# Kernel tuning notes

Hardware: AMD Instinct MI355X
Metric: run time of the kernel (lower is better)

The kernel has to match this reference:

```python
import jax, jax.numpy as jnp
import numpy as np

N = 50000
E = 800000
NFEAT, NHID, NCODE, NCLASS = 512, 256, 64, 40


def setup_inputs() -> dict:
    key = jax.random.key(0)
    ks = jax.random.split(key, 16)
    def glorot(k, shape):
        lim = 1.0 / np.sqrt(shape[0])
        return jax.random.uniform(k, shape, jnp.float32, -lim, lim)
    return {
        "x": jax.random.normal(ks[0], (N, NFEAT), jnp.float32),
        "edge_src": jax.random.randint(ks[1], (E,), 0, N, jnp.int32),
        "edge_dst": jax.random.randint(ks[2], (E,), 0, N, jnp.int32),
        "edge_weight": jax.random.uniform(ks[3], (E,), jnp.float32),
        "eps": jax.random.normal(ks[4], (N, NCODE), jnp.float32),
        # gc1: GraphConvolution(nfeat, nhid)
        "W1": glorot(ks[5], (NFEAT, NHID)),
        "b1": glorot(ks[6], (NHID,)),
        # fc11 / fc12: Linear(nhid, ncode)
        "W_mu": glorot(ks[7], (NHID, NCODE)),
        "b_mu": glorot(ks[8], (NCODE,)),
        "W_lv": glorot(ks[9], (NHID, NCODE)),
        "b_lv": glorot(ks[10], (NCODE,)),
        # fc2: Linear(ncode, nhid)
        "W_dec": glorot(ks[11], (NCODE, NHID)),
        "b_dec": glorot(ks[12], (NHID,)),
        # gc2: GraphConvolution(2*nhid, nclass)
        "W2": glorot(ks[13], (2 * NHID, NCLASS)),
        "b2": glorot(ks[14], (NCLASS,)),
    }


def spmm(edge_src, edge_dst, edge_weight, support):
    # spmm(adj, support): gather rows at src, scale by edge weight, scatter-add to dst
    msgs = support[edge_src] * edge_weight[:, None]  # [E, d]
    return jax.ops.segment_sum(msgs, edge_dst, num_segments=N)


def reference(x, edge_src, edge_dst, edge_weight, eps,
              W1, b1, W_mu, b_mu, W_lv, b_lv, W_dec, b_dec, W2, b2):
    # gc1: relu(spmm(adj, x @ W1) + b1)
    h1 = jax.nn.relu(spmm(edge_src, edge_dst, edge_weight, x @ W1) + b1)
    # dropout is identity in inference mode
    mu = h1 @ W_mu + b_mu
    log_var = h1 @ W_lv + b_lv
    # reparametrize: std = exp(log_var) (as in source, no 0.5 factor)
    z = mu + eps * jnp.exp(log_var)
    # decode
    x1 = jax.nn.relu(z @ W_dec + b_dec)
    x1 = jnp.concatenate([x1, h1], axis=1)  # [N, 2*nhid]
    # gc2
    logits = spmm(edge_src, edge_dst, edge_weight, x1 @ W2) + b2
    return jax.nn.log_softmax(logits, axis=1)
```

## Files before the change

kernel.cpp:

```cpp
#include <hip/hip_runtime.h>
#include <math.h>

#define N_NODES 50000
#define N_EDGES 800000
#define NFEAT 512
#define NHID 256
#define NCODE 64
#define NCLASS 40
#define NCLS_PAD 48
#define NB_SCAN 196

typedef __attribute__((ext_vector_type(8))) short short8;
typedef __attribute__((ext_vector_type(8))) unsigned short ushort8;
typedef __attribute__((ext_vector_type(4))) unsigned short ushort4v;
typedef __attribute__((ext_vector_type(4))) float floatx4;

__device__ inline unsigned short f2bf(float f) {
    unsigned u = __builtin_bit_cast(unsigned, f);
    u += 0x7fff + ((u >> 16) & 1);
    return (unsigned short)(u >> 16);
}
__device__ inline float bf2f(unsigned short h) {
    return __builtin_bit_cast(float, (unsigned)h << 16);
}

__global__ __launch_bounds__(256) void hist_kernel(const int* __restrict__ dst,
                                                   int* __restrict__ counts) {
    int t = blockIdx.x * 256 + threadIdx.x;
    if (t < N_EDGES) atomicAdd(&counts[dst[t]], 1);
}

__global__ __launch_bounds__(256) void scan_block_sums(const int* __restrict__ counts,
                                                       int* __restrict__ blockSums) {
    __shared__ int red[256];
    int t = threadIdx.x;
    int i = blockIdx.x * 256 + t;
    red[t] = (i < N_NODES) ? counts[i] : 0;
    __syncthreads();
#pragma unroll
    for (int off = 128; off > 0; off >>= 1) {
        if (t < off) red[t] += red[t + off];
        __syncthreads();
    }
    if (t == 0) blockSums[blockIdx.x] = red[0];
}

__global__ __launch_bounds__(256) void scan_block_offsets(const int* __restrict__ blockSums,
                                                          int* __restrict__ blockOffsets,
                                                          int* __restrict__ offsets) {
    __shared__ int s[256];
    int t = threadIdx.x;
    int v = (t < NB_SCAN) ? blockSums[t] : 0;
    s[t] = v;
    __syncthreads();
#pragma unroll
    for (int off = 1; off < 256; off <<= 1) {
        int x = (t >= off) ? s[t - off] : 0;
        __syncthreads();
        s[t] += x;
        __syncthreads();
    }
    if (t < NB_SCAN) blockOffsets[t] = s[t] - v;
    if (t == 255) offsets[N_NODES] = s[255];
}

__global__ __launch_bounds__(256) void scan_final(const int* __restrict__ counts,
                                                  const int* __restrict__ blockOffsets,
                                                  int* __restrict__ offsets) {
    __shared__ int s[256];
    int t = threadIdx.x;
    int i = blockIdx.x * 256 + t;
    int v = (i < N_NODES) ? counts[i] : 0;
    s[t] = v;
    __syncthreads();
#pragma unroll
    for (int off = 1; off < 256; off <<= 1) {
        int x = (t >= off) ? s[t - off] : 0;
        __syncthreads();
        s[t] += x;
        __syncthreads();
    }
    if (i < N_NODES) offsets[i] = blockOffsets[blockIdx.x] + s[t] - v;
}

__global__ __launch_bounds__(256) void scatter_kernel(const int* __restrict__ dst,
                                                      const int* __restrict__ src,
                                                      const float* __restrict__ w,
                                                      const int* __restrict__ offsets,
                                                      int* __restrict__ cursor,
                                                      int2* __restrict__ edges) {
    int t = blockIdx.x * 256 + threadIdx.x;
    if (t < N_EDGES) {
        int d = dst[t];
        int pos = offsets[d] + atomicAdd(&cursor[d], 1);
        edges[pos] = make_int2(src[t], __builtin_bit_cast(int, w[t]));
    }
}

__global__ __launch_bounds__(256) void wprep_kernel(const float* __restrict__ W1,
                                                    const float* __restrict__ W2,
                                                    const float* __restrict__ W_mu,
                                                    const float* __restrict__ W_lv,
                                                    const float* __restrict__ W_dec,
                                                    unsigned short* __restrict__ W1t,
                                                    unsigned short* __restrict__ W2bt,
                                                    unsigned short* __restrict__ W_mulvt,
                                                    unsigned short* __restrict__ W_dect) {
    int idx = blockIdx.x * 256 + threadIdx.x;
    if (idx < NFEAT * NHID) {
        int k = idx >> 8;
        int n = idx & 255;
        W1t[(size_t)n * NFEAT + k] = f2bf(W1[idx]);
    } else if (idx < NFEAT * NHID + NCLS_PAD * NFEAT) {
        int i2 = idx - NFEAT * NHID;
        int n = i2 >> 9;
        int k = i2 & 511;
        W2bt[i2] = (n < NCLASS) ? f2bf(W2[(size_t)k * NCLASS + n]) : (unsigned short)0;
    } else if (idx < NFEAT * NHID + NCLS_PAD * NFEAT + 128 * 256) {
        int i2 = idx - NFEAT * NHID - NCLS_PAD * NFEAT;
        int j = i2 >> 8;
        int k = i2 & 255;
        float v = (j < 64) ? W_mu[(size_t)k * NCODE + j] : W_lv[(size_t)k * NCODE + (j - 64)];
        W_mulvt[i2] = f2bf(v);
    } else if (idx < NFEAT * NHID + NCLS_PAD * NFEAT + 128 * 256 + 256 * 64) {
        int i2 = idx - NFEAT * NHID - NCLS_PAD * NFEAT - 128 * 256;
        int n = i2 >> 6;
        int k = i2 & 63;
        W_dect[i2] = f2bf(W_dec[(size_t)k * NHID + n]);
    }
}

__global__ __launch_bounds__(256) void gemm1_mfma(const float* __restrict__ A,
                                                  const unsigned short* __restrict__ Bt,
                                                  unsigned short* __restrict__ C) {
    __shared__ unsigned short As[64][72];
    __shared__ unsigned short Bs[128][72];
    int t = threadIdx.x;
    int wave = t >> 6, lane = t & 63;
    int quad = lane >> 4, m16 = lane & 15;
    int m0 = blockIdx.x * 64;
    int n0 = blockIdx.y * 128;

    floatx4 acc[8];
#pragma unroll
    for (int i = 0; i < 8; i++) acc[i] = (floatx4){0.f, 0.f, 0.f, 0.f};

    int ar = t >> 2;
    int ako = (t & 3) * 16;
    int arow = m0 + ar;
    if (arow >= N_NODES) arow = N_NODES - 1;
    const float* Abase = A + (size_t)arow * NFEAT + ako;

    int bcol = t >> 1;
    int bko = (t & 1) * 32;
    const unsigned short* Bbase = Bt + (size_t)(n0 + bcol) * NFEAT + bko;

    for (int k0 = 0; k0 < NFEAT; k0 += 64) {
        float4 a0 = *(const float4*)(Abase + k0);
        float4 a1 = *(const float4*)(Abase + k0 + 4);
        float4 a2 = *(const float4*)(Abase + k0 + 8);
        float4 a3 = *(const float4*)(Abase + k0 + 12);
        ushort8 b0 = *(const ushort8*)(Bbase + k0);
        ushort8 b1 = *(const ushort8*)(Bbase + k0 + 8);
        ushort8 b2 = *(const ushort8*)(Bbase + k0 + 16);
        ushort8 b3 = *(const ushort8*)(Bbase + k0 + 24);
        __syncthreads();
        ushort8 av0, av1;
        av0[0] = f2bf(a0.x); av0[1] = f2bf(a0.y); av0[2] = f2bf(a0.z); av0[3] = f2bf(a0.w);
        av0[4] = f2bf(a1.x); av0[5] = f2bf(a1.y); av0[6] = f2bf(a1.z); av0[7] = f2bf(a1.w);
        av1[0] = f2bf(a2.x); av1[1] = f2bf(a2.y); av1[2] = f2bf(a2.z); av1[3] = f2bf(a2.w);
        av1[4] = f2bf(a3.x); av1[5] = f2bf(a3.y); av1[6] = f2bf(a3.z); av1[7] = f2bf(a3.w);
        *(ushort8*)&As[ar][ako] = av0;
        *(ushort8*)&As[ar][ako + 8] = av1;
        *(ushort8*)&Bs[bcol][bko] = b0;
        *(ushort8*)&Bs[bcol][bko + 8] = b1;
        *(ushort8*)&Bs[bcol][bko + 16] = b2;
        *(ushort8*)&Bs[bcol][bko + 24] = b3;
        __syncthreads();
#pragma unroll
        for (int c = 0; c < 2; c++) {
            short8 afrag = *(const short8*)&As[wave * 16 + m16][c * 32 + quad * 8];
#pragma unroll
            for (int nt = 0; nt < 8; nt++) {
                short8 bfrag = *(const short8*)&Bs[nt * 16 + m16][c * 32 + quad * 8];
                acc[nt] = __builtin_amdgcn_mfma_f32_16x16x32_bf16(afrag, bfrag, acc[nt], 0, 0, 0);
            }
        }
    }
#pragma unroll
    for (int nt = 0; nt < 8; nt++) {
        int col = n0 + nt * 16 + m16;
#pragma unroll
        for (int r = 0; r < 4; r++) {
            int row = m0 + wave * 16 + quad * 4 + r;
            if (row < N_NODES) C[(size_t)row * NHID + col] = f2bf(acc[nt][r]);
        }
    }
}

__global__ __launch_bounds__(256) void spmm1_kernel(const int* __restrict__ offsets,
                                                    const int2* __restrict__ edges,
                                                    const unsigned short* __restrict__ S1b,
                                                    const float* __restrict__ b1,
                                                    unsigned short* __restrict__ x1cat) {
    int n = blockIdx.x * 4 + (threadIdx.x >> 6);
    int lane = threadIdx.x & 63;
    int beg = offsets[n], end = offsets[n + 1];
    float ax = 0.f, ay = 0.f, az = 0.f, aw = 0.f;
    int i = beg;
    for (; i + 8 <= end; i += 8) {
        int2 e[8];
        ushort4v r[8];
#pragma unroll
        for (int u = 0; u < 8; u++) e[u] = edges[i + u];
#pragma unroll
        for (int u = 0; u < 8; u++)
            r[u] = *(const ushort4v*)&S1b[(size_t)e[u].x * NHID + lane * 4];
#pragma unroll
        for (int u = 0; u < 8; u++) {
            float ww = __builtin_bit_cast(float, e[u].y);
            ax += ww * bf2f(r[u][0]);
            ay += ww * bf2f(r[u][1]);
            az += ww * bf2f(r[u][2]);
            aw += ww * bf2f(r[u][3]);
        }
    }
    for (; i < end; i++) {
        int2 e = edges[i];
        float ww = __builtin_bit_cast(float, e.y);
        ushort4v r = *(const ushort4v*)&S1b[(size_t)e.x * NHID + lane * 4];
        ax += ww * bf2f(r[0]); ay += ww * bf2f(r[1]);
        az += ww * bf2f(r[2]); aw += ww * bf2f(r[3]);
    }
    float4 bb = *(const float4*)&b1[lane * 4];
    ushort4v hb;
    hb[0] = f2bf(fmaxf(ax + bb.x, 0.f));
    hb[1] = f2bf(fmaxf(ay + bb.y, 0.f));
    hb[2] = f2bf(fmaxf(az + bb.z, 0.f));
    hb[3] = f2bf(fmaxf(aw + bb.w, 0.f));
    *(ushort4v*)&x1cat[(size_t)n * (2 * NHID) + NHID + lane * 4] = hb;
}

__global__ __launch_bounds__(256) void mlp_mfma(const unsigned short* __restrict__ x1cat_ro,
                                                const float* __restrict__ eps,
                                                const float* __restrict__ b_mu,
                                                const float* __restrict__ b_lv,
                                                const unsigned short* __restrict__ W_mulvt,
                                                const float* __restrict__ b_dec,
                                                const unsigned short* __restrict__ W_dect,
                                                unsigned short* __restrict__ x1cat) {
    __shared__ float smulv[16][132];
    __shared__ unsigned short z_bf[16][72];
    int t = threadIdx.x;
    int wave = t >> 6, lane = t & 63;
    int quad = lane >> 4, m16 = lane & 15;
    int node0 = blockIdx.x * 16;

    {
        floatx4 acc[2];
        acc[0] = (floatx4){0.f, 0.f, 0.f, 0.f};
        acc[1] = (floatx4){0.f, 0.f, 0.f, 0.f};
        const unsigned short* Abase =
            x1cat_ro + (size_t)(node0 + m16) * 512 + 256 + quad * 8;
        const unsigned short* Bb0 = W_mulvt + (size_t)(wave * 32 + m16) * 256 + quad * 8;
        const unsigned short* Bb1 = Bb0 + 16 * 256;
#pragma unroll
        for (int k0 = 0; k0 < 256; k0 += 32) {
            short8 afrag = *(const short8*)(Abase + k0);
            short8 bf0 = *(const short8*)(Bb0 + k0);
            short8 bf1 = *(const short8*)(Bb1 + k0);
            acc[0] = __builtin_amdgcn_mfma_f32_16x16x32_bf16(afrag, bf0, acc[0], 0, 0, 0);
            acc[1] = __builtin_amdgcn_mfma_f32_16x16x32_bf16(afrag, bf1, acc[1], 0, 0, 0);
        }
#pragma unroll
        for (int nt = 0; nt < 2; nt++) {
            int j = wave * 32 + nt * 16 + m16;
            float bias = (j < 64) ? b_mu[j] : b_lv[j - 64];
#pragma unroll
            for (int r = 0; r < 4; r++)
                smulv[quad * 4 + r][j] = acc[nt][r] + bias;
        }
    }
    __syncthreads();
#pragma unroll
    for (int r = 0; r < 4; r++) {
        int idx = t + r * 256;
        int n = idx >> 6, j = idx & 63;
        float z = smulv[n][j] + eps[(size_t)node0 * NCODE + idx] * expf(smulv[n][64 + j]);
        z_bf[n][j] = f2bf(z);
    }
    __syncthreads();
    {
        floatx4 acc[4];
#pragma unroll
        for (int i = 0; i < 4; i++) acc[i] = (floatx4){0.f, 0.f, 0.f, 0.f};
#pragma unroll
        for (int ks = 0; ks < 2; ks++) {
            int k0 = ks * 32;
            short8 afrag = *(const short8*)&z_bf[m16][k0 + quad * 8];
#pragma unroll
            for (int nt = 0; nt < 4; nt++) {
                int col = wave * 64 + nt * 16 + m16;
                short8 bfrag = *(const short8*)(W_dect + (size_t)col * 64 + k0 + quad * 8);
                acc[nt] = __builtin_amdgcn_mfma_f32_16x16x32_bf16(afrag, bfrag, acc[nt], 0, 0, 0);
            }
        }
#pragma unroll
        for (int nt = 0; nt < 4; nt++) {
            int col = wave * 64 + nt * 16 + m16;
            float bias = b_dec[col];
#pragma unroll
            for (int r = 0; r < 4; r++) {
                int node = node0 + quad * 4 + r;
                x1cat[(size_t)node * 512 + col] = f2bf(fmaxf(acc[nt][r] + bias, 0.f));
            }
        }
    }
}

__global__ __launch_bounds__(256) void gemm2_mfma(const unsigned short* __restrict__ Xb,
                                                  const unsigned short* __restrict__ Bt,
                                                  unsigned short* __restrict__ S2b) {
    __shared__ unsigned short As[64][40];
    __shared__ unsigned short Bs[48][40];
    int t = threadIdx.x;
    int wave = t >> 6, lane = t & 63;
    int quad = lane >> 4, m16 = lane & 15;
    int m0 = blockIdx.x * 64;

    floatx4 acc[3];
#pragma unroll
    for (int i = 0; i < 3; i++) acc[i] = (floatx4){0.f, 0.f, 0.f, 0.f};

    int ar = t >> 2;
    int ako = (t & 3) * 8;
    int arow = m0 + ar;
    if (arow >= N_NODES) arow = N_NODES - 1;
    const unsigned short* Abase = Xb + (size_t)arow * NFEAT + ako;
    const unsigned short* Bbase = Bt + (size_t)(t >> 2) * NFEAT + ako;
    bool bload = (t >> 2) < NCLS_PAD;

    ushort8 a0 = *(const ushort8*)(Abase);
    ushort8 b0;
    if (bload) b0 = *(const ushort8*)(Bbase);

    for (int k0 = 0; k0 < NFEAT; k0 += 32) {
        __syncthreads();
        *(ushort8*)&As[ar][ako] = a0;
        if (bload) *(ushort8*)&Bs[t >> 2][ako] = b0;
        __syncthreads();
        int kn = (k0 + 32 < NFEAT) ? (k0 + 32) : k0;
        a0 = *(const ushort8*)(Abase + kn);
        if (bload) b0 = *(const ushort8*)(Bbase + kn);
        short8 afrag = *(const short8*)&As[wave * 16 + m16][quad * 8];
#pragma unroll
        for (int nt = 0; nt < 3; nt++) {
            short8 bfrag = *(const short8*)&Bs[nt * 16 + m16][quad * 8];
            acc[nt] = __builtin_amdgcn_mfma_f32_16x16x32_bf16(afrag, bfrag, acc[nt], 0, 0, 0);
        }
    }
#pragma unroll
    for (int nt = 0; nt < 3; nt++) {
        int col = nt * 16 + m16;
        if (col < NCLASS) {
#pragma unroll
            for (int r = 0; r < 4; r++) {
                int row = m0 + wave * 16 + quad * 4 + r;
                if (row < N_NODES) S2b[(size_t)row * NCLASS + col] = f2bf(acc[nt][r]);
            }
        }
    }
}

__global__ __launch_bounds__(256) void spmm2_softmax_kernel(const int* __restrict__ offsets,
                                                            const int2* __restrict__ edges,
                                                            const unsigned short* __restrict__ S2b,
                                                            const float* __restrict__ b2,
                                                            float* __restrict__ out) {
    int wave = threadIdx.x >> 6;
    int lane = threadIdx.x & 63;
    int n = blockIdx.x * 4 + wave;
    int beg = offsets[n], end = offsets[n + 1];
    float acc = 0.f;
    int i = beg;
    for (; i + 4 <= end; i += 4) {
        int2 e0 = edges[i], e1 = edges[i + 1], e2 = edges[i + 2], e3 = edges[i + 3];
        float w0 = __builtin_bit_cast(float, e0.y);
        float w1 = __builtin_bit_cast(float, e1.y);
        float w2 = __builtin_bit_cast(float, e2.y);
        float w3 = __builtin_bit_cast(float, e3.y);
        if (lane < NCLASS) {
            float v0 = bf2f(S2b[(size_t)e0.x * NCLASS + lane]);
            float v1 = bf2f(S2b[(size_t)e1.x * NCLASS + lane]);
            float v2 = bf2f(S2b[(size_t)e2.x * NCLASS + lane]);
            float v3 = bf2f(S2b[(size_t)e3.x * NCLASS + lane]);
            acc += w0 * v0 + w1 * v1 + w2 * v2 + w3 * v3;
        }
    }
    for (; i < end; i++) {
        int2 e = edges[i];
        float ww = __builtin_bit_cast(float, e.y);
        if (lane < NCLASS) acc += ww * bf2f(S2b[(size_t)e.x * NCLASS + lane]);
    }
    float v = (lane < NCLASS) ? (acc + b2[lane]) : -INFINITY;
    float m = v;
#pragma unroll
    for (int off = 32; off > 0; off >>= 1) m = fmaxf(m, __shfl_xor(m, off));
    float ex = (lane < NCLASS) ? expf(v - m) : 0.f;
    float ssum = ex;
#pragma unroll
    for (int off = 32; off > 0; off >>= 1) ssum += __shfl_xor(ssum, off);
    if (lane < NCLASS) out[(size_t)n * NCLASS + lane] = v - m - logf(ssum);
}

extern "C" void kernel_launch(void* const* d_in, const int* in_sizes, int n_in,
                              void* d_out, int out_size, void* d_ws, size_t ws_size,
                              hipStream_t stream) {
    const float* x     = (const float*)d_in[0];
    const int*   esrc  = (const int*)d_in[1];
    const int*   edst  = (const int*)d_in[2];
    const float* ew    = (const float*)d_in[3];
    const float* eps   = (const float*)d_in[4];
    const float* W1    = (const float*)d_in[5];
    const float* b1    = (const float*)d_in[6];
    const float* W_mu  = (const float*)d_in[7];
    const float* b_mu  = (const float*)d_in[8];
    const float* W_lv  = (const float*)d_in[9];
    const float* b_lv  = (const float*)d_in[10];
    const float* W_dec = (const float*)d_in[11];
    const float* b_dec = (const float*)d_in[12];
    const float* W2    = (const float*)d_in[13];
    const float* b2    = (const float*)d_in[14];
    float* out = (float*)d_out;

    unsigned short* support1b = (unsigned short*)d_ws;
    unsigned short* x1cat = support1b + (size_t)N_NODES * NHID;
    unsigned short* S2b = x1cat + (size_t)N_NODES * 2 * NHID;
    unsigned short* W1t    = S2b + (size_t)N_NODES * NCLASS;
    unsigned short* W2bt   = W1t + (size_t)NHID * NFEAT;
    unsigned short* W_mulvt = W2bt + (size_t)NCLS_PAD * NFEAT;
    unsigned short* W_dect  = W_mulvt + 128 * 256;
    int*   counts   = (int*)(((size_t)(W_dect + 256 * 64) + 3) & ~(size_t)3);
    int*   cursor   = counts + N_NODES;
    int*   offsets  = cursor + N_NODES;
    int*   blockSums    = offsets + N_NODES + 1;
    int*   blockOffsets = blockSums + NB_SCAN;
    int2*  edges    = (int2*)(blockOffsets + NB_SCAN);
    edges = (int2*)(((size_t)edges + 7) & ~(size_t)7);
    size_t need = (size_t)((char*)(edges + N_EDGES) - (char*)d_ws);
    if (ws_size < need) return;

    hipMemsetAsync(counts, 0, 2 * N_NODES * sizeof(int), stream);
    hist_kernel<<<(N_EDGES + 255) / 256, 256, 0, stream>>>(edst, counts);
    scan_block_sums<<<NB_SCAN, 256, 0, stream>>>(counts, blockSums);
    scan_block_offsets<<<1, 256, 0, stream>>>(blockSums, blockOffsets, offsets);
    scan_final<<<NB_SCAN, 256, 0, stream>>>(counts, blockOffsets, offsets);
    scatter_kernel<<<(N_EDGES + 255) / 256, 256, 0, stream>>>(edst, esrc, ew, offsets, cursor,
                                                              edges);

    wprep_kernel<<<800, 256, 0, stream>>>(W1, W2, W_mu, W_lv, W_dec, W1t, W2bt, W_mulvt, W_dect);
    dim3 g1((N_NODES + 63) / 64, 2);
    gemm1_mfma<<<g1, 256, 0, stream>>>(x, W1t, support1b);
    spmm1_kernel<<<N_NODES / 4, 256, 0, stream>>>(offsets, edges, support1b, b1, x1cat);
    mlp_mfma<<<N_NODES / 16, 256, 0, stream>>>(x1cat, eps, b_mu, b_lv, W_mulvt, b_dec, W_dect,
                                               x1cat);
    gemm2_mfma<<<(N_NODES + 63) / 64, 256, 0, stream>>>(x1cat, W2bt, S2b);
    spmm2_softmax_kernel<<<N_NODES / 4, 256, 0, stream>>>(offsets, edges, S2b, b2, out);
}
```

Baseline: 452.7 us.

## Retile gemm1 to 128x128 double-buffered swizzled LDS, stage W2 fully in gemm2

gemm1 moves from a 64x128 tile to a 128x128 tile split into 2x2 wave sub-tiles with 4x4 MFMA accumulators each. It double-buffers LDS, loads B directly into LDS with global_load_lds, and converts A with packed bf16 conversion into an XOR-swizzled layout, so the tile has more reuse and global loads overlap with compute. gemm2 now stages the whole padded W2 into LDS once and reads A fragments straight from global memory, removing the per-step barriers. The cost is higher register and LDS use, which may lower occupancy.

```diff
diff --git a/kernel.cpp b/kernel.cpp
--- a/kernel.cpp
+++ b/kernel.cpp
@@ -22,6 +22,16 @@
 }
 __device__ inline float bf2f(unsigned short h) {
     return __builtin_bit_cast(float, (unsigned)h << 16);
+}
+__device__ inline unsigned pkbf(float lo, float hi) {
+    unsigned r;
+    asm("v_cvt_pk_bf16_f32 %0, %1, %2" : "=v"(r) : "v"(lo), "v"(hi));
+    return r;
+}
+__device__ inline void gload_lds16(const void* g, void* l) {
+    __builtin_amdgcn_global_load_lds(
+        (const __attribute__((address_space(1))) unsigned int*)g,
+        (__attribute__((address_space(3))) unsigned int*)l, 16, 0, 0);
 }
 
 __global__ __launch_bounds__(256) void hist_kernel(const int* __restrict__ dst,
@@ -133,67 +143,108 @@
 __global__ __launch_bounds__(256) void gemm1_mfma(const float* __restrict__ A,
                                                   const unsigned short* __restrict__ Bt,
                                                   unsigned short* __restrict__ C) {
-    __shared__ unsigned short As[64][72];
-    __shared__ unsigned short Bs[128][72];
+    __shared__ unsigned short As[2][128 * 64];
+    __shared__ unsigned short Bs[2][128 * 64];
     int t = threadIdx.x;
     int wave = t >> 6, lane = t & 63;
     int quad = lane >> 4, m16 = lane & 15;
-    int m0 = blockIdx.x * 64;
+    int wr = wave >> 1, wc = wave & 1;
+    int m0 = blockIdx.x * 128;
     int n0 = blockIdx.y * 128;
 
-    floatx4 acc[8];
-#pragma unroll
-    for (int i = 0; i < 8; i++) acc[i] = (floatx4){0.f, 0.f, 0.f, 0.f};
-
-    int ar = t >> 2;
-    int ako = (t & 3) * 16;
-    int arow = m0 + ar;
-    if (arow >= N_NODES) arow = N_NODES - 1;
-    const float* Abase = A + (size_t)arow * NFEAT + ako;
-
-    int bcol = t >> 1;
-    int bko = (t & 1) * 32;
-    const unsigned short* Bbase = Bt + (size_t)(n0 + bcol) * NFEAT + bko;
-
+    int srow = t >> 3;
+    int kcs = (t & 7) ^ (srow & 7);
+    const float* Ap[4];
+    const unsigned short* Bp[4];
+#pragma unroll
+    for (int r = 0; r < 4; ++r) {
+        int row = r * 32 + srow;
+        int ga = m0 + row;
+        if (ga >= N_NODES) ga = N_NODES - 1;
+        Ap[r] = A + (size_t)ga * NFEAT + kcs * 8;
+        Bp[r] = Bt + (size_t)(n0 + row) * NFEAT + kcs * 8;
+    }
+
+    floatx4 acc[4][4];
+#pragma unroll
+    for (int m = 0; m < 4; ++m)
+#pragma unroll
+        for (int n = 0; n < 4; ++n) acc[m][n] = (floatx4){0.f, 0.f, 0.f, 0.f};
+
+    float4 a0[4], a1[4];
+#pragma unroll
+    for (int r = 0; r < 4; ++r)
+        gload_lds16(Bp[r], &Bs[0][(r * 256 + wave * 64) * 8]);
+#pragma unroll
+    for (int r = 0; r < 4; ++r) {
+        a0[r] = *(const float4*)(Ap[r]);
+        a1[r] = *(const float4*)(Ap[r] + 4);
+    }
+#pragma unroll
+    for (int r = 0; r < 4; ++r) {
+        uint4 w;
+        w.x = pkbf(a0[r].x, a0[r].y);
+        w.y = pkbf(a0[r].z, a0[r].w);
+        w.z = pkbf(a1[r].x, a1[r].y);
+        w.w = pkbf(a1[r].z, a1[r].w);
+        *(uint4*)&As[0][(r * 256 + t) * 8] = w;
+    }
+    __syncthreads();
+
+#pragma unroll
     for (int k0 = 0; k0 < NFEAT; k0 += 64) {
-        float4 a0 = *(const float4*)(Abase + k0);
-        float4 a1 = *(const float4*)(Abase + k0 + 4);
-        float4 a2 = *(const float4*)(Abase + k0 + 8);
-        float4 a3 = *(const float4*)(Abase + k0 + 12);
-        ushort8 b0 = *(const ushort8*)(Bbase + k0);
-        ushort8 b1 = *(const ushort8*)(Bbase + k0 + 8);
-        ushort8 b2 = *(const ushort8*)(Bbase + k0 + 16);
-        ushort8 b3 = *(const ushort8*)(Bbase + k0 + 24);
-        __syncthreads();
-        ushort8 av0, av1;
-        av0[0] = f2bf(a0.x); av0[1] = f2bf(a0.y); av0[2] = f2bf(a0.z); av0[3] = f2bf(a0.w);
-        av0[4] = f2bf(a1.x); av0[5] = f2bf(a1.y); av0[6] = f2bf(a1.z); av0[7] = f2bf(a1.w);
-        av1[0] = f2bf(a2.x); av1[1] = f2bf(a2.y); av1[2] = f2bf(a2.z); av1[3] = f2bf(a2.w);
-        av1[4] = f2bf(a3.x); av1[5] = f2bf(a3.y); av1[6] = f2bf(a3.z); av1[7] = f2bf(a3.w);
-        *(ushort8*)&As[ar][ako] = av0;
-        *(ushort8*)&As[ar][ako + 8] = av1;
-        *(ushort8*)&Bs[bcol][bko] = b0;
-        *(ushort8*)&Bs[bcol][bko + 8] = b1;
-        *(ushort8*)&Bs[bcol][bko + 16] = b2;
-        *(ushort8*)&Bs[bcol][bko + 24] = b3;
-        __syncthreads();
-#pragma unroll
-        for (int c = 0; c < 2; c++) {
-            short8 afrag = *(const short8*)&As[wave * 16 + m16][c * 32 + quad * 8];
-#pragma unroll
-            for (int nt = 0; nt < 8; nt++) {
-                short8 bfrag = *(const short8*)&Bs[nt * 16 + m16][c * 32 + quad * 8];
-                acc[nt] = __builtin_amdgcn_mfma_f32_16x16x32_bf16(afrag, bfrag, acc[nt], 0, 0, 0);
+        const int cur = (k0 >> 6) & 1, nxt = cur ^ 1;
+        const bool more = (k0 + 64 < NFEAT);
+        if (more) {
+#pragma unroll
+            for (int r = 0; r < 4; ++r)
+                gload_lds16(Bp[r] + (k0 + 64), &Bs[nxt][(r * 256 + wave * 64) * 8]);
+#pragma unroll
+            for (int r = 0; r < 4; ++r) {
+                a0[r] = *(const float4*)(Ap[r] + k0 + 64);
+                a1[r] = *(const float4*)(Ap[r] + k0 + 68);
             }
         }
-    }
-#pragma unroll
-    for (int nt = 0; nt < 8; nt++) {
-        int col = n0 + nt * 16 + m16;
-#pragma unroll
-        for (int r = 0; r < 4; r++) {
-            int row = m0 + wave * 16 + quad * 4 + r;
-            if (row < N_NODES) C[(size_t)row * NHID + col] = f2bf(acc[nt][r]);
+#pragma unroll
+        for (int c = 0; c < 2; ++c) {
+            int sw = ((c * 4 + quad) ^ (m16 & 7)) * 8;
+            short8 af[4], bfr[4];
+#pragma unroll
+            for (int m = 0; m < 4; ++m)
+                af[m] = *(const short8*)&As[cur][(wr * 64 + m * 16 + m16) * 64 + sw];
+#pragma unroll
+            for (int n = 0; n < 4; ++n)
+                bfr[n] = *(const short8*)&Bs[cur][(wc * 64 + n * 16 + m16) * 64 + sw];
+#pragma unroll
+            for (int m = 0; m < 4; ++m)
+#pragma unroll
+                for (int n = 0; n < 4; ++n)
+                    acc[m][n] =
+                        __builtin_amdgcn_mfma_f32_16x16x32_bf16(af[m], bfr[n], acc[m][n], 0, 0, 0);
+        }
+        if (more) {
+#pragma unroll
+            for (int r = 0; r < 4; ++r) {
+                uint4 w;
+                w.x = pkbf(a0[r].x, a0[r].y);
+                w.y = pkbf(a0[r].z, a0[r].w);
+                w.z = pkbf(a1[r].x, a1[r].y);
+                w.w = pkbf(a1[r].z, a1[r].w);
+                *(uint4*)&As[nxt][(r * 256 + t) * 8] = w;
+            }
+            __syncthreads();
+        }
+    }
+#pragma unroll
+    for (int m = 0; m < 4; ++m) {
+#pragma unroll
+        for (int n = 0; n < 4; ++n) {
+            int col = n0 + wc * 64 + n * 16 + m16;
+#pragma unroll
+            for (int r = 0; r < 4; ++r) {
+                int row = m0 + wr * 64 + m * 16 + quad * 4 + r;
+                if (row < N_NODES) C[(size_t)row * NHID + col] = f2bf(acc[m][n][r]);
+            }
         }
     }
 }
@@ -321,42 +372,35 @@
 __global__ __launch_bounds__(256) void gemm2_mfma(const unsigned short* __restrict__ Xb,
                                                   const unsigned short* __restrict__ Bt,
                                                   unsigned short* __restrict__ S2b) {
-    __shared__ unsigned short As[64][40];
-    __shared__ unsigned short Bs[48][40];
+    __shared__ unsigned short Bs[NCLS_PAD][520];
     int t = threadIdx.x;
     int wave = t >> 6, lane = t & 63;
     int quad = lane >> 4, m16 = lane & 15;
     int m0 = blockIdx.x * 64;
 
+#pragma unroll
+    for (int r = 0; r < 12; ++r) {
+        int cidx = r * 256 + t;
+        int row = cidx >> 6, col = (cidx & 63) * 8;
+        *(ushort8*)&Bs[row][col] = *(const ushort8*)&Bt[(size_t)row * NFEAT + col];
+    }
+
+    int arow = m0 + wave * 16 + m16;
+    if (arow >= N_NODES) arow = N_NODES - 1;
+    const unsigned short* Abase = Xb + (size_t)arow * NFEAT + quad * 8;
+
     floatx4 acc[3];
 #pragma unroll
     for (int i = 0; i < 3; i++) acc[i] = (floatx4){0.f, 0.f, 0.f, 0.f};
-
-    int ar = t >> 2;
-    int ako = (t & 3) * 8;
-    int arow = m0 + ar;
-    if (arow >= N_NODES) arow = N_NODES - 1;
-    const unsigned short* Abase = Xb + (size_t)arow * NFEAT + ako;
-    const unsigned short* Bbase = Bt + (size_t)(t >> 2) * NFEAT + ako;
-    bool bload = (t >> 2) < NCLS_PAD;
-
-    ushort8 a0 = *(const ushort8*)(Abase);
-    ushort8 b0;
-    if (bload) b0 = *(const ushort8*)(Bbase);
-
+    __syncthreads();
+
+#pragma unroll
     for (int k0 = 0; k0 < NFEAT; k0 += 32) {
-        __syncthreads();
-        *(ushort8*)&As[ar][ako] = a0;
-        if (bload) *(ushort8*)&Bs[t >> 2][ako] = b0;
-        __syncthreads();
-        int kn = (k0 + 32 < NFEAT) ? (k0 + 32) : k0;
-        a0 = *(const ushort8*)(Abase + kn);
-        if (bload) b0 = *(const ushort8*)(Bbase + kn);
-        short8 afrag = *(const short8*)&As[wave * 16 + m16][quad * 8];
+        short8 af = *(const short8*)(Abase + k0);
 #pragma unroll
         for (int nt = 0; nt < 3; nt++) {
-            short8 bfrag = *(const short8*)&Bs[nt * 16 + m16][quad * 8];
-            acc[nt] = __builtin_amdgcn_mfma_f32_16x16x32_bf16(afrag, bfrag, acc[nt], 0, 0, 0);
+            short8 bfr = *(const short8*)&Bs[nt * 16 + m16][k0 + quad * 8];
+            acc[nt] = __builtin_amdgcn_mfma_f32_16x16x32_bf16(af, bfr, acc[nt], 0, 0, 0);
         }
     }
 #pragma unroll
@@ -459,7 +503,7 @@
                                                               edges);
 
     wprep_kernel<<<800, 256, 0, stream>>>(W1, W2, W_mu, W_lv, W_dec, W1t, W2bt, W_mulvt, W_dect);
-    dim3 g1((N_NODES + 63) / 64, 2);
+    dim3 g1((N_NODES + 127) / 128, 2);
     gemm1_mfma<<<g1, 256, 0, stream>>>(x, W1t, support1b);
     spmm1_kernel<<<N_NODES / 4, 256, 0, stream>>>(offsets, edges, support1b, b1, x1cat);
     mlp_mfma<<<N_NODES / 16, 256, 0, stream>>>(x1cat, eps, b_mu, b_lv, W_mulvt, b_dec, W_dect,
```

Measured after the change: 454.4 us. About the same (+0.4%).
